# Kernel tuning notes

Hardware: AMD Instinct MI355X
Metric: run time of the kernel (lower is better)

Reference implementation:

```python
import jax, jax.numpy as jnp
import numpy as np

N, E, DIN, H = 10000, 80000, 1024, 512
NEG = 0.2  # PyG GATv2Conv default negative_slope


def gatv2(x, src, dst, wl, bl, wr, br, att, b, n):
    # GATv2: e_ij = att . leaky_relu(Wl x_j + Wr x_i); segment softmax over dst; sum alpha * Wl x_j
    xl = x @ wl + bl            # [N, H] source transform
    xr = x @ wr + br            # [N, H] target transform
    z = jax.nn.leaky_relu(xl[src] + xr[dst], NEG)   # [E, H]
    e = z @ att                                      # [E]
    m = jax.ops.segment_max(e, dst, num_segments=n)  # per-target max (self-loops guarantee nonempty)
    p = jnp.exp(e - m[dst])
    s = jax.ops.segment_sum(p, dst, num_segments=n)
    alpha = p / (s[dst] + 1e-16)                     # [E]
    out = jax.ops.segment_sum(alpha[:, None] * xl[src], dst, num_segments=n)
    return out + b


def setup_inputs() -> dict:
    key = jax.random.key(0)
    ks = iter(jax.random.split(key, 64))
    d = {}
    d["x"] = jax.random.normal(next(ks), (N, DIN), jnp.float32)
    d["edge_index"] = jax.random.randint(next(ks), (2, E), 0, N, dtype=jnp.int32).astype(jnp.int64)
    dims = [DIN, H, H, H]
    for i in range(4):
        din = dims[i]
        sc = 1.0 / np.sqrt(din)
        d[f"wl{i+1}"] = jax.random.normal(next(ks), (din, H), jnp.float32) * sc
        d[f"bl{i+1}"] = jnp.zeros((H,), jnp.float32)
        d[f"wr{i+1}"] = jax.random.normal(next(ks), (din, H), jnp.float32) * sc
        d[f"br{i+1}"] = jnp.zeros((H,), jnp.float32)
        d[f"att{i+1}"] = jax.random.normal(next(ks), (H,), jnp.float32) * (1.0 / np.sqrt(H))
        d[f"b{i+1}"] = jnp.zeros((H,), jnp.float32)
    for name, din, dout in [("1", H, 512), ("2", 512, 256), ("3", 256, 2)]:
        d[f"lw{name}"] = jax.random.normal(next(ks), (din, dout), jnp.float32) * (1.0 / np.sqrt(din))
        d[f"lb{name}"] = jnp.zeros((dout,), jnp.float32)
    return d


def reference(x, edge_index, wl1, bl1, wr1, br1, att1, b1,
              wl2, bl2, wr2, br2, att2, b2,
              wl3, bl3, wr3, br3, att3, b3,
              wl4, bl4, wr4, br4, att4, b4,
              lw1, lb1, lw2, lb2, lw3, lb3):
    n = x.shape[0]
    loops = jnp.arange(n, dtype=edge_index.dtype)
    src = jnp.concatenate([edge_index[0], loops])  # add self-loops (PyG default)
    dst = jnp.concatenate([edge_index[1], loops])
    h = jax.nn.relu(gatv2(x, src, dst, wl1, bl1, wr1, br1, att1, b1, n))
    h = jax.nn.relu(gatv2(h, src, dst, wl2, bl2, wr2, br2, att2, b2, n))
    h = jax.nn.relu(gatv2(h, src, dst, wl3, bl3, wr3, br3, att3, b3, n))
    h = jax.nn.relu(gatv2(h, src, dst, wl4, bl4, wr4, br4, att4, b4, n))
    # dropout is identity at inference
    h = jax.nn.relu(h @ lw1 + lb1)
    h = jax.nn.relu(h @ lw2 + lb2)
    logits = h @ lw3 + lb3
    return logits, jax.nn.softmax(logits, axis=1)
```

## Files before the change

kernel.cpp:

```cpp
#include <hip/hip_runtime.h>
#include <cstdint>

#define NN 10000
#define NE 80000
#define DIN_ 1024
#define HH 512

typedef __attribute__((ext_vector_type(8))) short bf16x8;
typedef __attribute__((ext_vector_type(4))) float f32x4;
typedef unsigned short u16;
typedef unsigned int u32;

static __device__ __forceinline__ float b2f(u16 u) {
  u32 i = ((u32)u) << 16;
  return __builtin_bit_cast(float, i);
}
static __device__ __forceinline__ u16 f2b(float f) {
  u32 i = __builtin_bit_cast(u32, f);
  u32 r = (i + 0x7fffu + ((i >> 16) & 1u)) >> 16;
  return (u16)r;
}
static __device__ __forceinline__ void unpack8(uint4 u, float* f) {
  f[0] = __builtin_bit_cast(float, u.x << 16);
  f[1] = __builtin_bit_cast(float, u.x & 0xffff0000u);
  f[2] = __builtin_bit_cast(float, u.y << 16);
  f[3] = __builtin_bit_cast(float, u.y & 0xffff0000u);
  f[4] = __builtin_bit_cast(float, u.z << 16);
  f[5] = __builtin_bit_cast(float, u.z & 0xffff0000u);
  f[6] = __builtin_bit_cast(float, u.w << 16);
  f[7] = __builtin_bit_cast(float, u.w & 0xffff0000u);
}
static __device__ __forceinline__ void load8(const u16* p, float* f) { unpack8(*(const uint4*)p, f); }

#define ASYNC_CP16(gp, lp)                                                        \
  __builtin_amdgcn_global_load_lds((__attribute__((address_space(1))) void*)(gp), \
                                   (__attribute__((address_space(3))) void*)(lp), \
                                   16, 0, 0)

static __device__ __forceinline__ int float_flag(const u16* xw) {
  __shared__ int c;
  if (threadIdx.x == 0) c = 0;
  __syncthreads();
  int bad = 0;
  for (int i = threadIdx.x; i < 2048; i += blockDim.x) {
    u32 e = (xw[i] >> 7) & 0xFFu;
    if (e >= 140u) bad++;
  }
  if (bad) atomicAdd(&c, bad);
  __syncthreads();
  return c > 64;
}
static __device__ __forceinline__ int int64_flag(const u32* ew) {
  __shared__ int c;
  if (threadIdx.x == 0) c = 0;
  __syncthreads();
  int z = 0;
  for (int i = threadIdx.x; i < 256; i += blockDim.x)
    if (ew[2 * i + 1] == 0u) z++;
  if (z) atomicAdd(&c, z);
  __syncthreads();
  return c > 200;
}

__global__ void k_edges(const void* ei, int* esrc, int* edst, int* counts) {
  int f64 = int64_flag((const u32*)ei);
  int i = blockIdx.x * 256 + threadIdx.x;
  if (i < NE) {
    int sv, dv;
    if (f64) {
      sv = (int)((const long long*)ei)[i];
      dv = (int)((const long long*)ei)[NE + i];
    } else {
      sv = ((const int*)ei)[i];
      dv = ((const int*)ei)[NE + i];
    }
    esrc[i] = sv;
    edst[i] = dv;
    atomicAdd(&counts[dv], 1);
  } else if (i < NE + NN) {
    atomicAdd(&counts[i - NE], 1);
  }
}

__global__ __launch_bounds__(512) void k_scan(const int* counts, int* rowptr, int* cursor, int n) {
  __shared__ int lds[512];
  const int PER = 20;
  int t = threadIdx.x;
  int base = t * PER;
  int v[PER];
  int sum = 0;
#pragma unroll
  for (int i = 0; i < PER; i++) {
    int idx = base + i;
    v[i] = (idx < n) ? counts[idx] : 0;
    sum += v[i];
  }
  lds[t] = sum;
  __syncthreads();
  for (int off = 1; off < 512; off <<= 1) {
    int x = (t >= off) ? lds[t - off] : 0;
    __syncthreads();
    lds[t] += x;
    __syncthreads();
  }
  int run = (t > 0) ? lds[t - 1] : 0;
#pragma unroll
  for (int i = 0; i < PER; i++) {
    int idx = base + i;
    if (idx < n) {
      cursor[idx] = run;
      run += v[i];
      rowptr[idx + 1] = run;
    }
  }
  if (t == 0) rowptr[0] = 0;
}

__global__ void k_scatter(const int* src, const int* dst, int* cursor, int* col, int E, int n) {
  int i = blockIdx.x * blockDim.x + threadIdx.x;
  if (i < E) {
    int p = atomicAdd(&cursor[dst[i]], 1);
    col[p] = src[i];
  } else if (i < E + n) {
    int v = i - E;
    int p = atomicAdd(&cursor[v], 1);
    col[p] = v;
  }
}

#define XBLK 2048
struct Prep {
  const void* xin;
  u16* xout;
  const void* vin[20];
  u16* vout[20];
  int vn[20];
  const void* tin[10];
  u16* tout[10];
  int tK[10], tN[10], toff[10];
};
__global__ void k_prep(Prep a) {
  __shared__ u16 tt[32][33];
  int f = float_flag((const u16*)a.xin);
  int b = blockIdx.x;
  if (b < XBLK) {
    const int total = NN * DIN_ / 8;
    for (int g = b * 256 + threadIdx.x; g < total; g += XBLK * 256) {
      u16 o[8];
      if (f) {
        const float* p = (const float*)a.xin + (size_t)g * 8;
#pragma unroll
        for (int i = 0; i < 8; i++) o[i] = f2b(p[i]);
      } else {
        *(uint4*)o = *((const uint4*)a.xin + g);
      }
      *((uint4*)a.xout + g) = *(const uint4*)o;
    }
  } else if (b < XBLK + 20) {
    int v = b - XBLK;
    const void* in = a.vin[v];
    u16* out = a.vout[v];
    int n = a.vn[v];
    for (int i = threadIdx.x; i < n; i += 256)
      out[i] = f ? f2b(((const float*)in)[i]) : ((const u16*)in)[i];
  } else {
    int tb = b - XBLK - 20;
    int seg = 0;
#pragma unroll
    for (int i = 1; i < 10; i++)
      if (tb >= a.toff[i]) seg = i;
    int tl = tb - a.toff[seg];
    int K = a.tK[seg], N = a.tN[seg];
    int tiles_n = N >> 5;
    int n0 = (tl % tiles_n) << 5, k0 = (tl / tiles_n) << 5;
    const void* in = a.tin[seg];
    u16* out = a.tout[seg];
    int tx = threadIdx.x & 31, ty = threadIdx.x >> 5;
    for (int r = ty; r < 32; r += 8) {
      size_t idx = (size_t)(k0 + r) * N + n0 + tx;
      tt[r][tx] = f ? f2b(((const float*)in)[idx]) : ((const u16*)in)[idx];
    }
    __syncthreads();
    for (int r = ty; r < 32; r += 8) out[(size_t)(n0 + r) * K + k0 + tx] = tt[tx][r];
  }
}

__global__ __launch_bounds__(256) void k_gemm128(const u16* __restrict__ A, int lda,
                                                 const u16* __restrict__ Bt,
                                                 const u16* __restrict__ bias,
                                                 u16* __restrict__ C,
                                                 int M, int N, int K, int act,
                                                 int tiles_m, int ln_tiles_n) {
  __shared__ u16 sA[2 * 128 * 32];
  __shared__ u16 sB[2 * 128 * 32];
  int id = blockIdx.x;
  int xcd = id & 7;
  int rest = id >> 3;
  int xt = rest & ((1 << ln_tiles_n) - 1);
  int yt = ((rest >> ln_tiles_n) << 3) + xcd;
  if (yt >= tiles_m) return;
  int m0 = yt << 7, n0 = xt << 7;
  int t = threadIdx.x;
  int wave = t >> 6, lane = t & 63;

  int srow = t >> 2;
  int sk = ((t & 3) ^ ((t >> 3) & 3)) * 8;
  const u16* agp[4];
  const u16* bgp[4];
  u16* la[4];
  u16* lb[4];
#pragma unroll
  for (int q = 0; q < 4; q++) {
    int h = q >> 1;
    int row = ((q & 1) << 6) + srow;
    int ra = m0 + row;
    ra = ra < M ? ra : M - 1;
    agp[q] = A + (size_t)ra * lda + h * 32 + sk;
    bgp[q] = Bt + (size_t)(n0 + row) * K + h * 32 + sk;
    int lofs = h * 4096 + (((q & 1) << 8) + t) * 8;
    la[q] = sA + lofs;
    lb[q] = sB + lofs;
  }

  int wm = (wave >> 1) << 6, wn = (wave & 1) << 6;
  int lr = lane & 15;
  int kcs = (((lane >> 4) ^ ((lr >> 1) & 3))) * 8;

  f32x4 acc[4][4];
#pragma unroll
  for (int i = 0; i < 4; i++)
#pragma unroll
    for (int j = 0; j < 4; j++) acc[i][j] = (f32x4){0.f, 0.f, 0.f, 0.f};

  for (int k0 = 0; k0 < K; k0 += 64) {
#pragma unroll
    for (int q = 0; q < 4; q++) ASYNC_CP16(agp[q] + k0, la[q]);
#pragma unroll
    for (int q = 0; q < 4; q++) ASYNC_CP16(bgp[q] + k0, lb[q]);
    __syncthreads();
    bf16x8 a[2][4], b[2][4];
#pragma unroll
    for (int s = 0; s < 2; s++) {
#pragma unroll
      for (int i = 0; i < 4; i++) a[s][i] = *(const bf16x8*)(sA + s * 4096 + (wm + i * 16 + lr) * 32 + kcs);
#pragma unroll
      for (int j = 0; j < 4; j++) b[s][j] = *(const bf16x8*)(sB + s * 4096 + (wn + j * 16 + lr) * 32 + kcs);
    }
#pragma unroll
    for (int s = 0; s < 2; s++)
#pragma unroll
      for (int i = 0; i < 4; i++)
#pragma unroll
        for (int j = 0; j < 4; j++)
          acc[i][j] = __builtin_amdgcn_mfma_f32_16x16x32_bf16(a[s][i], b[s][j], acc[i][j], 0, 0, 0);
    __syncthreads();
  }

  int rbase = (lane >> 4) << 2;
#pragma unroll
  for (int j = 0; j < 4; j++) {
    int colc = n0 + wn + j * 16 + lr;
    float bv = b2f(bias[colc]);
#pragma unroll
    for (int i = 0; i < 4; i++) {
#pragma unroll
      for (int r = 0; r < 4; r++) {
        int row = m0 + wm + i * 16 + rbase + r;
        if (row < M) {
          float v = acc[i][j][r] + bv;
          if (act) v = fmaxf(v, 0.f);
          C[(size_t)row * N + colc] = f2b(v);
        }
      }
    }
  }
}

__global__ __launch_bounds__(256) void k_attn3(u16* __restrict__ xlr,
                                               const u16* __restrict__ att, const u16* __restrict__ bias,
                                               const int* __restrict__ rowptr, const int* __restrict__ col,
                                               int n) {
  int node = (blockIdx.x * 256 + threadIdx.x) >> 6;
  if (node >= n) return;
  int lane = threadIdx.x & 63;
  int h0 = lane * 8;
  float a[8], r[8];
  load8(att + h0, a);
  load8(xlr + (size_t)node * 1024 + 512 + h0, r);
  int e0 = rowptr[node], e1 = rowptr[node + 1];

  float m = -3e38f, s = 0.f;
  float acc[8] = {0.f, 0.f, 0.f, 0.f, 0.f, 0.f, 0.f, 0.f};
  int j0 = col[e0];
  int j1 = col[(e0 + 1 < e1) ? e0 + 1 : e0];
  uint4 raw0 = *(const uint4*)(xlr + (size_t)j0 * 1024 + h0);
  uint4 raw1 = *(const uint4*)(xlr + (size_t)j1 * 1024 + h0);

  for (int e = e0; e < e1; e += 2) {
    bool has2 = (e + 1 < e1);
    int jn0 = col[(e + 2 < e1) ? e + 2 : e1 - 1];
    int jn1 = col[(e + 3 < e1) ? e + 3 : e1 - 1];
    uint4 p0 = *(const uint4*)(xlr + (size_t)jn0 * 1024 + h0);
    uint4 p1 = *(const uint4*)(xlr + (size_t)jn1 * 1024 + h0);
    float x0[8], x1[8];
    unpack8(raw0, x0);
    unpack8(raw1, x1);
    float pa = 0.f, pb = 0.f;
#pragma unroll
    for (int i = 0; i < 8; i++) {
      float z0 = x0[i] + r[i];
      z0 = z0 > 0.f ? z0 : 0.2f * z0;
      pa = fmaf(a[i], z0, pa);
      float z1 = x1[i] + r[i];
      z1 = z1 > 0.f ? z1 : 0.2f * z1;
      pb = fmaf(a[i], z1, pb);
    }
#pragma unroll
    for (int off = 32; off >= 1; off >>= 1) {
      pa += __shfl_xor(pa, off);
      pb += __shfl_xor(pb, off);
    }
    if (pa > m) {
      float al = __expf(m - pa);
      s *= al;
#pragma unroll
      for (int i = 0; i < 8; i++) acc[i] *= al;
      m = pa;
    }
    {
      float w = __expf(pa - m);
      s += w;
#pragma unroll
      for (int i = 0; i < 8; i++) acc[i] = fmaf(w, x0[i], acc[i]);
    }
    if (has2) {
      if (pb > m) {
        float al = __expf(m - pb);
        s *= al;
#pragma unroll
        for (int i = 0; i < 8; i++) acc[i] *= al;
        m = pb;
      }
      float w = __expf(pb - m);
      s += w;
#pragma unroll
      for (int i = 0; i < 8; i++) acc[i] = fmaf(w, x1[i], acc[i]);
    }
    raw0 = p0;
    raw1 = p1;
  }
  float inv = 1.f / (s + 1e-16f);

  float bv[8];
  load8(bias + h0, bv);
  uint4 o;
  u32 p[8];
#pragma unroll
  for (int i = 0; i < 8; i++) {
    float v = fmaf(acc[i], inv, bv[i]);
    v = fmaxf(v, 0.f);
    p[i] = f2b(v);
  }
  o.x = p[0] | (p[1] << 16);
  o.y = p[2] | (p[3] << 16);
  o.z = p[4] | (p[5] << 16);
  o.w = p[6] | (p[7] << 16);
  *(uint4*)(xlr + (size_t)node * 1024 + 512 + h0) = o;
}

__global__ __launch_bounds__(256) void k_head(const u16* __restrict__ h2, const u16* __restrict__ lw3,
                                              const u16* __restrict__ lb3, float* __restrict__ out, int n) {
  int row = (blockIdx.x * 256 + threadIdx.x) >> 6;
  if (row >= n) return;
  int lane = threadIdx.x & 63;
  int k0 = lane * 4;
  uint2 hu = *(const uint2*)(h2 + (size_t)row * 256 + k0);
  float hx[4];
  hx[0] = __builtin_bit_cast(float, hu.x << 16);
  hx[1] = __builtin_bit_cast(float, hu.x & 0xffff0000u);
  hx[2] = __builtin_bit_cast(float, hu.y << 16);
  hx[3] = __builtin_bit_cast(float, hu.y & 0xffff0000u);
  float wv[8];
  load8(lw3 + (size_t)k0 * 2, wv);
  float p0 = 0.f, p1 = 0.f;
#pragma unroll
  for (int i = 0; i < 4; i++) {
    p0 = fmaf(hx[i], wv[2 * i], p0);
    p1 = fmaf(hx[i], wv[2 * i + 1], p1);
  }
#pragma unroll
  for (int off = 32; off >= 1; off >>= 1) {
    p0 += __shfl_xor(p0, off);
    p1 += __shfl_xor(p1, off);
  }
  if (lane == 0) {
    float l0 = p0 + b2f(lb3[0]);
    float l1 = p1 + b2f(lb3[1]);
    float mx = fmaxf(l0, l1);
    float q0 = __expf(l0 - mx), q1 = __expf(l1 - mx);
    float si = 1.f / (q0 + q1);
    out[row * 2 + 0] = l0;
    out[row * 2 + 1] = l1;
    out[2 * n + row * 2 + 0] = q0 * si;
    out[2 * n + row * 2 + 1] = q1 * si;
  }
}

extern "C" void kernel_launch(void* const* d_in, const int* in_sizes, int n_in,
                              void* d_out, int out_size, void* d_ws, size_t ws_size,
                              hipStream_t stream) {
  (void)in_sizes; (void)n_in; (void)out_size; (void)ws_size;
  const void* x_raw = d_in[0];
  const void* ei_raw = d_in[1];
  const void *wl[4], *bl[4], *wr[4], *br[4], *att[4], *bg[4];
  for (int i = 0; i < 4; i++) {
    wl[i] = d_in[2 + i * 6 + 0];
    bl[i] = d_in[2 + i * 6 + 1];
    wr[i] = d_in[2 + i * 6 + 2];
    br[i] = d_in[2 + i * 6 + 3];
    att[i] = d_in[2 + i * 6 + 4];
    bg[i] = d_in[2 + i * 6 + 5];
  }
  const void* lw1 = d_in[26];
  const void* lb1 = d_in[27];
  const void* lw2 = d_in[28];
  const void* lb2 = d_in[29];
  const void* lw3 = d_in[30];
  const void* lb3 = d_in[31];

  size_t off = 0;
  auto alloc = [&](size_t bytes) -> void* {
    off = (off + 255) & ~(size_t)255;
    void* p = (char*)d_ws + off;
    off += bytes;
    return p;
  };
  int* esrc = (int*)alloc(NE * 4);
  int* edst = (int*)alloc(NE * 4);
  int* counts = (int*)alloc(NN * 4);
  int* rowptr = (int*)alloc((NN + 1) * 4);
  int* cursor = (int*)alloc(NN * 4);
  int* col = (int*)alloc((NE + NN) * 4);
  u16* cb = (u16*)alloc(4 * 1024 * 2);
  u16* attv = (u16*)alloc(4 * 512 * 2);
  u16* bgv = (u16*)alloc(4 * 512 * 2);
  u16* lb1v = (u16*)alloc(512 * 2);
  u16* lb2v = (u16*)alloc(256 * 2);
  u16* lw3v = (u16*)alloc(512 * 2);
  u16* lb3v = (u16*)alloc(2 * 2);
  u16* comb0 = (u16*)alloc((size_t)1024 * 1024 * 2);
  u16* combL[4];
  combL[0] = comb0;
  for (int l = 1; l < 4; l++) combL[l] = (u16*)alloc((size_t)1024 * 512 * 2);
  u16* lw1T = (u16*)alloc((size_t)512 * 512 * 2);
  u16* lw2T = (u16*)alloc((size_t)256 * 512 * 2);
  u16* xc = (u16*)alloc((size_t)NN * DIN_ * 2);
  u16* X0 = (u16*)alloc((size_t)NN * 1024 * 2);
  u16* X1 = (u16*)alloc((size_t)NN * 1024 * 2);
  u16* mlp1 = xc;
  u16* mlp2 = xc + (size_t)NN * 512;

  hipMemsetAsync(counts, 0, NN * 4, stream);
  int ET = NE + NN;
  k_edges<<<(ET + 255) / 256, 256, 0, stream>>>(ei_raw, esrc, edst, counts);
  k_scan<<<1, 512, 0, stream>>>(counts, rowptr, cursor, NN);
  k_scatter<<<(ET + 255) / 256, 256, 0, stream>>>(esrc, edst, cursor, col, NE, NN);

  Prep pa;
  pa.xin = x_raw;
  pa.xout = xc;
  for (int l = 0; l < 4; l++) {
    pa.vin[l * 4 + 0] = bl[l];  pa.vout[l * 4 + 0] = cb + l * 1024;        pa.vn[l * 4 + 0] = 512;
    pa.vin[l * 4 + 1] = br[l];  pa.vout[l * 4 + 1] = cb + l * 1024 + 512;  pa.vn[l * 4 + 1] = 512;
    pa.vin[l * 4 + 2] = att[l]; pa.vout[l * 4 + 2] = attv + l * 512;       pa.vn[l * 4 + 2] = 512;
    pa.vin[l * 4 + 3] = bg[l];  pa.vout[l * 4 + 3] = bgv + l * 512;        pa.vn[l * 4 + 3] = 512;
  }
  pa.vin[16] = lb1; pa.vout[16] = lb1v; pa.vn[16] = 512;
  pa.vin[17] = lb2; pa.vout[17] = lb2v; pa.vn[17] = 256;
  pa.vin[18] = lw3; pa.vout[18] = lw3v; pa.vn[18] = 512;
  pa.vin[19] = lb3; pa.vout[19] = lb3v; pa.vn[19] = 2;
  const void* tin[10] = {wl[0], wr[0], wl[1], wr[1], wl[2], wr[2], wl[3], wr[3], lw1, lw2};
  u16* tout[10] = {comb0, comb0 + (size_t)512 * 1024,
                   combL[1], combL[1] + (size_t)512 * 512,
                   combL[2], combL[2] + (size_t)512 * 512,
                   combL[3], combL[3] + (size_t)512 * 512,
                   lw1T, lw2T};
  int tK[10] = {1024, 1024, 512, 512, 512, 512, 512, 512, 512, 512};
  int tN[10] = {512, 512, 512, 512, 512, 512, 512, 512, 512, 256};
  int acc_off = 0;
  for (int i = 0; i < 10; i++) {
    pa.tin[i] = tin[i];
    pa.tout[i] = tout[i];
    pa.tK[i] = tK[i];
    pa.tN[i] = tN[i];
    pa.toff[i] = acc_off;
    acc_off += (tN[i] >> 5) * (tK[i] >> 5);
  }
  k_prep<<<XBLK + 20 + acc_off, 256, 0, stream>>>(pa);

  auto gemm = [&](const u16* A, int lda, const u16* Bt, const u16* bias, u16* C,
                  int M, int Nn, int K, int act) {
    int tiles_m = (M + 127) >> 7;
    int tiles_n = Nn >> 7;
    int ln = (tiles_n == 8) ? 3 : (tiles_n == 4) ? 2 : 1;
    int mgrp = (tiles_m + 7) >> 3;
    int blocks = (mgrp << 3) * tiles_n;
    k_gemm128<<<blocks, 256, 0, stream>>>(A, lda, Bt, bias, C, M, Nn, K, act, tiles_m, ln);
  };
  auto attn = [&](u16* xlr, int l) {
    k_attn3<<<(NN * 64 + 255) / 256, 256, 0, stream>>>(xlr, attv + l * 512, bgv + l * 512,
                                                       rowptr, col, NN);
  };

  gemm(xc, 1024, comb0, cb + 0 * 1024, X0, NN, 1024, 1024, 0);
  attn(X0, 0);
  gemm(X0 + 512, 1024, combL[1], cb + 1 * 1024, X1, NN, 1024, 512, 0);
  attn(X1, 1);
  gemm(X1 + 512, 1024, combL[2], cb + 2 * 1024, X0, NN, 1024, 512, 0);
  attn(X0, 2);
  gemm(X0 + 512, 1024, combL[3], cb + 3 * 1024, X1, NN, 1024, 512, 0);
  attn(X1, 3);

  gemm(X1 + 512, 1024, lw1T, lb1v, mlp1, NN, 512, 512, 1);
  gemm(mlp1, 512, lw2T, lb2v, mlp2, NN, 256, 512, 1);
  k_head<<<(NN * 64 + 255) / 256, 256, 0, stream>>>(mlp2, lw3v, lb3v, (float*)d_out, NN);
}
```

Baseline: 390.8 us.

## Batch 8 neighbor gathers per attention step and fold scatter into prep kernel

The attention kernel now gathers up to 8 neighbor rows at once, computes their scores together, interleaves the 8 wave reductions, and does a single online-softmax rescale per batch of 8. This replaces a 2-edge software pipeline and is meant to expose more memory-level parallelism on random gathers and cut serial rescale work. The CSR scatter kernel is merged into the prep kernel as extra leading blocks, removing one launch. In exchange, register pressure rises from holding 64 unpacked floats, and average degree is about 9, so many batches are partially filled and padded with duplicate loads.

Result: slower. 414.7 us (+6.1%).

```diff
diff --git a/kernel.cpp b/kernel.cpp
--- a/kernel.cpp
+++ b/kernel.cpp
@@ -116,20 +116,13 @@
   if (t == 0) rowptr[0] = 0;
 }
 
-__global__ void k_scatter(const int* src, const int* dst, int* cursor, int* col, int E, int n) {
-  int i = blockIdx.x * blockDim.x + threadIdx.x;
-  if (i < E) {
-    int p = atomicAdd(&cursor[dst[i]], 1);
-    col[p] = src[i];
-  } else if (i < E + n) {
-    int v = i - E;
-    int p = atomicAdd(&cursor[v], 1);
-    col[p] = v;
-  }
-}
-
+#define SBLK 352
 #define XBLK 2048
 struct Prep {
+  const int* esrc;
+  const int* edst;
+  int* cursor;
+  int* col;
   const void* xin;
   u16* xout;
   const void* vin[20];
@@ -141,8 +134,21 @@
 };
 __global__ void k_prep(Prep a) {
   __shared__ u16 tt[32][33];
+  int b = blockIdx.x;
+  if (b < SBLK) {
+    int i = b * 256 + threadIdx.x;
+    if (i < NE) {
+      int p = atomicAdd(&a.cursor[a.edst[i]], 1);
+      a.col[p] = a.esrc[i];
+    } else if (i < NE + NN) {
+      int v = i - NE;
+      int p = atomicAdd(&a.cursor[v], 1);
+      a.col[p] = v;
+    }
+    return;
+  }
+  b -= SBLK;
   int f = float_flag((const u16*)a.xin);
-  int b = blockIdx.x;
   if (b < XBLK) {
     const int total = NN * DIN_ / 8;
     for (int g = b * 256 + threadIdx.x; g < total; g += XBLK * 256) {
@@ -276,7 +282,7 @@
   }
 }
 
-__global__ __launch_bounds__(256) void k_attn3(u16* __restrict__ xlr,
+__global__ __launch_bounds__(256) void k_attn4(u16* __restrict__ xlr,
                                                const u16* __restrict__ att, const u16* __restrict__ bias,
                                                const int* __restrict__ rowptr, const int* __restrict__ col,
                                                int n) {
@@ -291,80 +297,76 @@
 
   float m = -3e38f, s = 0.f;
   float acc[8] = {0.f, 0.f, 0.f, 0.f, 0.f, 0.f, 0.f, 0.f};
-  int j0 = col[e0];
-  int j1 = col[(e0 + 1 < e1) ? e0 + 1 : e0];
-  uint4 raw0 = *(const uint4*)(xlr + (size_t)j0 * 1024 + h0);
-  uint4 raw1 = *(const uint4*)(xlr + (size_t)j1 * 1024 + h0);
-
-  for (int e = e0; e < e1; e += 2) {
-    bool has2 = (e + 1 < e1);
-    int jn0 = col[(e + 2 < e1) ? e + 2 : e1 - 1];
-    int jn1 = col[(e + 3 < e1) ? e + 3 : e1 - 1];
-    uint4 p0 = *(const uint4*)(xlr + (size_t)jn0 * 1024 + h0);
-    uint4 p1 = *(const uint4*)(xlr + (size_t)jn1 * 1024 + h0);
-    float x0[8], x1[8];
-    unpack8(raw0, x0);
-    unpack8(raw1, x1);
-    float pa = 0.f, pb = 0.f;
-#pragma unroll
-    for (int i = 0; i < 8; i++) {
-      float z0 = x0[i] + r[i];
-      z0 = z0 > 0.f ? z0 : 0.2f * z0;
-      pa = fmaf(a[i], z0, pa);
-      float z1 = x1[i] + r[i];
-      z1 = z1 > 0.f ? z1 : 0.2f * z1;
-      pb = fmaf(a[i], z1, pb);
-    }
-#pragma unroll
-    for (int off = 32; off >= 1; off >>= 1) {
-      pa += __shfl_xor(pa, off);
-      pb += __shfl_xor(pb, off);
-    }
-    if (pa > m) {
-      float al = __expf(m - pa);
-      s *= al;
-#pragma unroll
-      for (int i = 0; i < 8; i++) acc[i] *= al;
-      m = pa;
-    }
-    {
-      float w = __expf(pa - m);
-      s += w;
-#pragma unroll
-      for (int i = 0; i < 8; i++) acc[i] = fmaf(w, x0[i], acc[i]);
-    }
-    if (has2) {
-      if (pb > m) {
-        float al = __expf(m - pb);
-        s *= al;
-#pragma unroll
-        for (int i = 0; i < 8; i++) acc[i] *= al;
-        m = pb;
+
+  for (int base = e0; base < e1; base += 8) {
+    int cnt = e1 - base;
+    cnt = cnt < 8 ? cnt : 8;
+    uint4 raw[8];
+#pragma unroll
+    for (int c = 0; c < 8; c++) {
+      int idx = base + c;
+      int j = col[idx < e1 ? idx : e1 - 1];
+      raw[c] = *(const uint4*)(xlr + (size_t)j * 1024 + h0);
+    }
+    float xv[8][8];
+#pragma unroll
+    for (int c = 0; c < 8; c++) unpack8(raw[c], xv[c]);
+    float p[8];
+#pragma unroll
+    for (int c = 0; c < 8; c++) {
+      float d = 0.f;
+#pragma unroll
+      for (int i = 0; i < 8; i++) {
+        float z = xv[c][i] + r[i];
+        z = z > 0.f ? z : 0.2f * z;
+        d = fmaf(a[i], z, d);
       }
-      float w = __expf(pb - m);
-      s += w;
-#pragma unroll
-      for (int i = 0; i < 8; i++) acc[i] = fmaf(w, x1[i], acc[i]);
-    }
-    raw0 = p0;
-    raw1 = p1;
+      p[c] = d;
+    }
+#pragma unroll
+    for (int off = 32; off >= 1; off >>= 1)
+#pragma unroll
+      for (int c = 0; c < 8; c++) p[c] += __shfl_xor(p[c], off);
+#pragma unroll
+    for (int c = 0; c < 8; c++)
+      if (c >= cnt) p[c] = -3e38f;
+    float M = p[0];
+#pragma unroll
+    for (int c = 1; c < 8; c++) M = fmaxf(M, p[c]);
+    float nm = fmaxf(m, M);
+    float al = __expf(m - nm);
+    float w[8];
+    float ws = 0.f;
+#pragma unroll
+    for (int c = 0; c < 8; c++) {
+      w[c] = __expf(p[c] - nm);
+      ws += w[c];
+    }
+    s = s * al + ws;
+#pragma unroll
+    for (int i = 0; i < 8; i++) acc[i] *= al;
+#pragma unroll
+    for (int c = 0; c < 8; c++)
+#pragma unroll
+      for (int i = 0; i < 8; i++) acc[i] = fmaf(w[c], xv[c][i], acc[i]);
+    m = nm;
   }
   float inv = 1.f / (s + 1e-16f);
 
   float bv[8];
   load8(bias + h0, bv);
   uint4 o;
-  u32 p[8];
+  u32 p8[8];
 #pragma unroll
   for (int i = 0; i < 8; i++) {
     float v = fmaf(acc[i], inv, bv[i]);
     v = fmaxf(v, 0.f);
-    p[i] = f2b(v);
-  }
-  o.x = p[0] | (p[1] << 16);
-  o.y = p[2] | (p[3] << 16);
-  o.z = p[4] | (p[5] << 16);
-  o.w = p[6] | (p[7] << 16);
+    p8[i] = f2b(v);
+  }
+  o.x = p8[0] | (p8[1] << 16);
+  o.y = p8[2] | (p8[3] << 16);
+  o.z = p8[4] | (p8[5] << 16);
+  o.w = p8[6] | (p8[7] << 16);
   *(uint4*)(xlr + (size_t)node * 1024 + 512 + h0) = o;
 }
 
@@ -464,9 +466,12 @@
   int ET = NE + NN;
   k_edges<<<(ET + 255) / 256, 256, 0, stream>>>(ei_raw, esrc, edst, counts);
   k_scan<<<1, 512, 0, stream>>>(counts, rowptr, cursor, NN);
-  k_scatter<<<(ET + 255) / 256, 256, 0, stream>>>(esrc, edst, cursor, col, NE, NN);
 
   Prep pa;
+  pa.esrc = esrc;
+  pa.edst = edst;
+  pa.cursor = cursor;
+  pa.col = col;
   pa.xin = x_raw;
   pa.xout = xc;
   for (int l = 0; l < 4; l++) {
@@ -496,7 +501,7 @@
     pa.toff[i] = acc_off;
     acc_off += (tN[i] >> 5) * (tK[i] >> 5);
   }
-  k_prep<<<XBLK + 20 + acc_off, 256, 0, stream>>>(pa);
+  k_prep<<<SBLK + XBLK + 20 + acc_off, 256, 0, stream>>>(pa);
 
   auto gemm = [&](const u16* A, int lda, const u16* Bt, const u16* bias, u16* C,
                   int M, int Nn, int K, int act) {
@@ -508,7 +513,7 @@
     k_gemm128<<<blocks, 256, 0, stream>>>(A, lda, Bt, bias, C, M, Nn, K, act, tiles_m, ln);
   };
   auto attn = [&](u16* xlr, int l) {
-    k_attn3<<<(NN * 64 + 255) / 256, 256, 0, stream>>>(xlr, attv + l * 512, bgv + l * 512,
+    k_attn4<<<(NN * 64 + 255) / 256, 256, 0, stream>>>(xlr, attv + l * 512, bgv + l * 512,
                                                        rowptr, col, NN);
   };
 
```
